# Performance work log

Measured on AMD Instinct MI355X. Metric: run time of the kernel, lower is better.

## Reference

```python
import jax, jax.numpy as jnp
import numpy as np

E, D, H, T = 8, 2048, 5632, 32768  # experts, dim, hidden_dim, total routed tokens


def setup_inputs() -> dict:
    key = jax.random.key(0)
    k_x, k1, k2, k3 = jax.random.split(key, 4)
    x = jax.random.normal(k_x, (T, D), dtype=jnp.float32)
    # trunc_normal init stds per init_weights (approx: plain normal, same scale)
    std = (2.0 / (D * 24)) ** 0.5
    w1 = jax.random.normal(k1, (E, H, D), dtype=jnp.float32) * std
    w2 = jax.random.normal(k2, (E, D, H), dtype=jnp.float32) * std
    w3 = jax.random.normal(k3, (E, H, D), dtype=jnp.float32) * std
    # tokens are pre-sorted by expert; even split 4096 tokens/expert (sums to T)
    num_tokens_per_expert = jnp.full((E,), T // E, dtype=jnp.int32)
    return {"x": x, "w1": w1, "w2": w2, "w3": w3,
            "num_tokens_per_expert": num_tokens_per_expert}


def _grouped_experts(x, w1, w2, w3, counts):
    # Faithful to _run_experts_grouped_mm: grouped GEMMs computed in bf16,
    # SwiGLU activation, cast back to x dtype.
    xb = x.astype(jnp.bfloat16)
    w1b = jnp.transpose(w1.astype(jnp.bfloat16), (0, 2, 1))  # [E, D, H]
    w3b = jnp.transpose(w3.astype(jnp.bfloat16), (0, 2, 1))  # [E, D, H]
    w2b = jnp.transpose(w2.astype(jnp.bfloat16), (0, 2, 1))  # [E, H, D]
    h1 = jax.lax.ragged_dot(xb, w1b, counts)   # [T, H]
    h3 = jax.lax.ragged_dot(xb, w3b, counts)   # [T, H]
    h = jax.nn.silu(h1) * h3                   # fused SwiGLU gate
    out = jax.lax.ragged_dot(h, w2b, counts)   # [T, D]
    return out.astype(x.dtype)


def reference(x, w1, w2, w3, num_tokens_per_expert):
    return _grouped_experts(x, w1, w2, w3, num_tokens_per_expert)
```

## Files before the change

kernel.cpp:

```cpp
#include <hip/hip_runtime.h>
#include <hip/hip_bf16.h>
#include <stdint.h>

#define TT 32768
#define DD 2048
#define HH 5632
#define NE 8

typedef __bf16 bf16;
typedef __bf16 bf16x8 __attribute__((ext_vector_type(8)));
typedef float  f32x4  __attribute__((ext_vector_type(4)));

__device__ __forceinline__ void gl16(const void* g, void* l) {
    __builtin_amdgcn_global_load_lds(
        (const __attribute__((address_space(1))) void*)g,
        (__attribute__((address_space(3))) void*)l, 16, 0, 0);
}
#define VMW(n) asm volatile("s_waitcnt vmcnt(" #n ")" ::: "memory")
#define LGKM0() do { asm volatile("s_waitcnt lgkmcnt(0)" ::: "memory"); \
                     __builtin_amdgcn_sched_barrier(0); } while (0)
#define BARRIER() __builtin_amdgcn_s_barrier()

__device__ __forceinline__ int swz(int off) { return off ^ (((off >> 7) & 3) << 4); }

__device__ __forceinline__ int expert_of(const int* counts, int row0) {
    int base = 0;
    for (int i = 0; i < NE; ++i) { int c = counts[i]; if (row0 < base + c) return i; base += c; }
    return NE - 1;
}

__global__ __launch_bounds__(256)
void k_cvt(const float* __restrict__ in, bf16* __restrict__ out, long n) {
    long i = ((long)blockIdx.x * 256 + threadIdx.x) * 8;
    const long stride = (long)gridDim.x * 256 * 8;
    for (; i < n; i += stride) {
        const float4* p = (const float4*)(in + i);
        float4 a = p[0], b = p[1];
        union { bf16 v[8]; uint4 u; } r;
        r.v[0] = (bf16)a.x; r.v[1] = (bf16)a.y; r.v[2] = (bf16)a.z; r.v[3] = (bf16)a.w;
        r.v[4] = (bf16)b.x; r.v[5] = (bf16)b.y; r.v[6] = (bf16)b.z; r.v[7] = (bf16)b.w;
        *(uint4*)(out + i) = r.u;
    }
}

__global__ __launch_bounds__(512, 2)
void k_moe1(const bf16* __restrict__ xb, const bf16* __restrict__ w1b,
            const bf16* __restrict__ w3b, const int* __restrict__ counts,
            bf16* __restrict__ h) {
    extern __shared__ __align__(16) char sm[];
    const int tid = threadIdx.x;
    const int c = blockIdx.x & 7;
    const int j = blockIdx.x >> 3;
    const int NSEG = 22;

    const int mt = (c << 4) + (j & 15);
    const int row0 = mt * 256;
    const int e = expert_of(counts, row0);

    const int s0 = swz(tid * 16);
    const int s1 = 8192 + s0;
    const int dst0 = tid * 16;

    const char* sa0 = (const char*)xb + (((size_t)(row0 + (s0 >> 6)) * DD) << 1) + (s0 & 63);
    const char* sa1 = (const char*)xb + (((size_t)(row0 + (s1 >> 6)) * DD) << 1) + (s1 & 63);
    const char* w1p = (const char*)(w1b + (size_t)e * HH * DD);
    const char* w3p = (const char*)(w3b + (size_t)e * HH * DD);
    int c0 = (j >> 4) * 128;
    const char* sa2 = w1p + (((size_t)(c0 + (s0 >> 6)) * DD) << 1) + (s0 & 63);
    const char* sa3 = w3p + (((size_t)(c0 + (s0 >> 6)) * DD) << 1) + (s0 & 63);
    const size_t WADV = ((size_t)256 * DD) << 1;

    auto stageA = [&](int ko, int bufb) {
        gl16(sa0 + ko, sm + bufb + dst0);
        gl16(sa1 + ko, sm + bufb + 8192 + dst0);
    };
    auto stageB = [&](int ko, int bufb) {
        gl16(sa2 + ko, sm + bufb + 16384 + dst0);
        gl16(sa3 + ko, sm + bufb + 24576 + dst0);
    };

    const int lane = tid & 63, wv = tid >> 6;
    const int wrow = wv >> 2, wcol = wv & 3;
    const int lrow = lane & 15, kb = (lane >> 4) << 4;
    const int aoff0 = swz((wrow * 128 + lrow) * 64 + kb);
    const int boff0 = swz((wcol * 32 + lrow) * 64 + kb);

    f32x4 acc1[8][2] = {};
    f32x4 acc3[8][2] = {};

    stageA(0, 0);          stageB(0, 0);
    stageA(64, 1 << 15);   stageB(64, 1 << 15);
    stageA(128, 2 << 15);  stageB(128, 2 << 15);
    VMW(8);
    BARRIER();

    int ccol0 = (j >> 4) * 128;
    const int crow = row0 + wrow * 128 + ((lane >> 4) << 2);

    for (int sg = 0; sg < NSEG; ++sg) {
        const bool fin = (sg == NSEG - 1);
        for (int tp = 0; tp < 16; ++tp) {
#pragma unroll
            for (int k = 0; k < 4; ++k) {
                const int t = tp * 4 + k;
                const char* db = sm + (k << 15);
                const int bS = ((k + 3) & 3) << 15;
                const int ko3 = ((t + 3) & 63) << 6;
                bf16x8 af[4], b1[2], b3[2];
#pragma unroll
                for (int mi = 0; mi < 4; ++mi) af[mi] = *(const bf16x8*)(db + aoff0 + mi * 1024);
#pragma unroll
                for (int ni = 0; ni < 2; ++ni) {
                    b1[ni] = *(const bf16x8*)(db + 16384 + boff0 + ni * 1024);
                    b3[ni] = *(const bf16x8*)(db + 24576 + boff0 + ni * 1024);
                }
                if (t == 61 && !fin) { sa2 += WADV; sa3 += WADV; }
                if (!fin || t < 61) stageA(ko3, bS);
                BARRIER();
                LGKM0();
                __builtin_amdgcn_s_setprio(1);
#pragma unroll
                for (int mi = 0; mi < 4; ++mi)
#pragma unroll
                    for (int ni = 0; ni < 2; ++ni) {
                        acc1[mi][ni] = __builtin_amdgcn_mfma_f32_16x16x32_bf16(af[mi], b1[ni], acc1[mi][ni], 0, 0, 0);
                        acc3[mi][ni] = __builtin_amdgcn_mfma_f32_16x16x32_bf16(af[mi], b3[ni], acc3[mi][ni], 0, 0, 0);
                    }
                __builtin_amdgcn_s_setprio(0);
                BARRIER();
                bf16x8 ag[4];
#pragma unroll
                for (int mi = 0; mi < 4; ++mi) ag[mi] = *(const bf16x8*)(db + aoff0 + (mi + 4) * 1024);
                if (!fin || t < 61) { stageB(ko3, bS); VMW(8); }
                else if (t == 61) { VMW(4); }
                else if (t == 62) { VMW(0); }
                BARRIER();
                LGKM0();
                __builtin_amdgcn_s_setprio(1);
#pragma unroll
                for (int mi = 0; mi < 4; ++mi)
#pragma unroll
                    for (int ni = 0; ni < 2; ++ni) {
                        acc1[mi + 4][ni] = __builtin_amdgcn_mfma_f32_16x16x32_bf16(ag[mi], b1[ni], acc1[mi + 4][ni], 0, 0, 0);
                        acc3[mi + 4][ni] = __builtin_amdgcn_mfma_f32_16x16x32_bf16(ag[mi], b3[ni], acc3[mi + 4][ni], 0, 0, 0);
                    }
                __builtin_amdgcn_s_setprio(0);
                BARRIER();
            }
        }
#pragma unroll
        for (int mi = 0; mi < 8; ++mi)
#pragma unroll
            for (int ni = 0; ni < 2; ++ni) {
#pragma unroll
                for (int jj = 0; jj < 4; ++jj) {
                    int row = crow + mi * 16 + jj;
                    int col = ccol0 + wcol * 32 + ni * 16 + lrow;
                    float f1 = (float)(bf16)acc1[mi][ni][jj];
                    float f3 = (float)(bf16)acc3[mi][ni][jj];
                    float s = f1 / (1.0f + __expf(-f1));
                    h[(size_t)row * HH + col] = (bf16)(s * f3);
                }
                acc1[mi][ni] = (f32x4){0.f, 0.f, 0.f, 0.f};
                acc3[mi][ni] = (f32x4){0.f, 0.f, 0.f, 0.f};
            }
        ccol0 += 256;
    }
}

__global__ __launch_bounds__(512, 2)
void k_g2(const bf16* __restrict__ hb, const bf16* __restrict__ w2b,
          const int* __restrict__ counts, float* __restrict__ out) {
    extern __shared__ __align__(16) char sm[];
    const int tid = threadIdx.x;
    const int c = blockIdx.x & 7;
    const int j = blockIdx.x >> 3;
    const int NSEG = 4;
    const int NT = 176;

    const int mt = (c << 4) + (j & 15);
    const int row0 = mt * 256;
    const int e = expert_of(counts, row0);

    const int s0 = swz(tid * 16);
    const int s1 = 8192 + s0;
    const int dst0 = tid * 16;

    const char* sa0 = (const char*)hb + (((size_t)(row0 + (s0 >> 6)) * HH) << 1) + (s0 & 63);
    const char* sa1 = (const char*)hb + (((size_t)(row0 + (s1 >> 6)) * HH) << 1) + (s1 & 63);
    const char* wp = (const char*)(w2b + (size_t)e * DD * HH);
    int c0 = (j >> 4) * 256;
    const char* sa2 = wp + (((size_t)(c0 + (s0 >> 6)) * HH) << 1) + (s0 & 63);
    const char* sa3 = wp + (((size_t)(c0 + (s1 >> 6)) * HH) << 1) + (s1 & 63);
    const size_t WADV = ((size_t)512 * HH) << 1;

    auto stageA = [&](int ko, int bufb) {
        gl16(sa0 + ko, sm + bufb + dst0);
        gl16(sa1 + ko, sm + bufb + 8192 + dst0);
    };
    auto stageB = [&](int ko, int bufb) {
        gl16(sa2 + ko, sm + bufb + 16384 + dst0);
        gl16(sa3 + ko, sm + bufb + 24576 + dst0);
    };

    const int lane = tid & 63, wv = tid >> 6;
    const int wrow = wv >> 2, wcol = wv & 3;
    const int lrow = lane & 15, kb = (lane >> 4) << 4;
    const int aoff0 = swz((wrow * 128 + lrow) * 64 + kb);
    const int boff0 = swz((wcol * 64 + lrow) * 64 + kb);

    f32x4 acc[8][4] = {};

    stageA(0, 0);          stageB(0, 0);
    stageA(64, 1 << 15);   stageB(64, 1 << 15);
    stageA(128, 2 << 15);  stageB(128, 2 << 15);
    VMW(8);
    BARRIER();

    int ccol0 = (j >> 4) * 256;
    const int crow = row0 + wrow * 128 + ((lane >> 4) << 2);

    for (int sg = 0; sg < NSEG; ++sg) {
        const bool fin = (sg == NSEG - 1);
        for (int tp = 0; tp < 44; ++tp) {
#pragma unroll
            for (int k = 0; k < 4; ++k) {
                const int t = tp * 4 + k;
                const char* db = sm + (k << 15);
                const int bS = ((k + 3) & 3) << 15;
                const int t3 = (t + 3 >= NT) ? t + 3 - NT : t + 3;
                const int ko3 = t3 << 6;
                bf16x8 af[4], bf[4];
#pragma unroll
                for (int mi = 0; mi < 4; ++mi) af[mi] = *(const bf16x8*)(db + aoff0 + mi * 1024);
#pragma unroll
                for (int ni = 0; ni < 4; ++ni) bf[ni] = *(const bf16x8*)(db + 16384 + boff0 + ni * 1024);
                if (t == NT - 3 && !fin) { sa2 += WADV; sa3 += WADV; }
                if (!fin || t < NT - 3) stageA(ko3, bS);
                BARRIER();
                LGKM0();
                __builtin_amdgcn_s_setprio(1);
#pragma unroll
                for (int mi = 0; mi < 4; ++mi)
#pragma unroll
                    for (int ni = 0; ni < 4; ++ni)
                        acc[mi][ni] = __builtin_amdgcn_mfma_f32_16x16x32_bf16(af[mi], bf[ni], acc[mi][ni], 0, 0, 0);
                __builtin_amdgcn_s_setprio(0);
                BARRIER();
                bf16x8 ag[4];
#pragma unroll
                for (int mi = 0; mi < 4; ++mi) ag[mi] = *(const bf16x8*)(db + aoff0 + (mi + 4) * 1024);
                if (!fin || t < NT - 3) { stageB(ko3, bS); VMW(8); }
                else if (t == NT - 3) { VMW(4); }
                else if (t == NT - 2) { VMW(0); }
                BARRIER();
                LGKM0();
                __builtin_amdgcn_s_setprio(1);
#pragma unroll
                for (int mi = 0; mi < 4; ++mi)
#pragma unroll
                    for (int ni = 0; ni < 4; ++ni)
                        acc[mi + 4][ni] = __builtin_amdgcn_mfma_f32_16x16x32_bf16(ag[mi], bf[ni], acc[mi + 4][ni], 0, 0, 0);
                __builtin_amdgcn_s_setprio(0);
                BARRIER();
            }
        }
#pragma unroll
        for (int mi = 0; mi < 8; ++mi)
#pragma unroll
            for (int ni = 0; ni < 4; ++ni) {
#pragma unroll
                for (int jj = 0; jj < 4; ++jj) {
                    int row = crow + mi * 16 + jj;
                    int col = ccol0 + wcol * 64 + ni * 16 + lrow;
                    out[(size_t)row * DD + col] = (float)(bf16)acc[mi][ni][jj];
                }
                acc[mi][ni] = (f32x4){0.f, 0.f, 0.f, 0.f};
            }
        ccol0 += 512;
    }
}

extern "C" void kernel_launch(void* const* d_in, const int* in_sizes, int n_in,
                              void* d_out, int out_size, void* d_ws, size_t ws_size,
                              hipStream_t stream) {
    const float* x      = (const float*)d_in[0];
    const float* w1     = (const float*)d_in[1];
    const float* w2     = (const float*)d_in[2];
    const float* w3     = (const float*)d_in[3];
    const int*   counts = (const int*)d_in[4];
    float* out = (float*)d_out;

    const size_t xb_b = (size_t)TT * DD * 2;
    const size_t h_b  = (size_t)TT * HH * 2;
    const size_t w_b  = (size_t)NE * HH * DD * 2;
    const size_t need_full = xb_b + h_b + 2 * w_b;
    if (ws_size < need_full) return;

    bf16* xb  = (bf16*)d_ws;
    bf16* h   = (bf16*)((char*)d_ws + xb_b);
    bf16* wsA = (bf16*)((char*)d_ws + xb_b + h_b);
    bf16* wsB = (bf16*)((char*)d_ws + xb_b + h_b + w_b);

    hipFuncSetAttribute((const void*)k_moe1, hipFuncAttributeMaxDynamicSharedMemorySize, 131072);
    hipFuncSetAttribute((const void*)k_g2,   hipFuncAttributeMaxDynamicSharedMemorySize, 131072);

    k_cvt<<<2048, 256, 0, stream>>>(x,  xb,  (long)TT * DD);
    k_cvt<<<2048, 256, 0, stream>>>(w1, wsA, (long)NE * HH * DD);
    k_cvt<<<2048, 256, 0, stream>>>(w3, wsB, (long)NE * HH * DD);
    k_moe1<<<256, 512, 131072, stream>>>(xb, wsA, wsB, counts, h);
    k_cvt<<<2048, 256, 0, stream>>>(w2, wsA, (long)NE * DD * HH);
    k_g2<<<256, 512, 131072, stream>>>(h, wsA, counts, out);
}
```

Measured before the change: 2.582 ms.

## Fuse w1/w3 fp32-to-bf16 conversion into first GEMM's B-tile staging

Removes the two separate conversion kernels for w1 and w3. The first grouped GEMM now loads fp32 weights into registers two k-steps ahead, converts them to bf16 and writes them into LDS, replacing direct global-to-LDS bf16 loads. This avoids writing and re-reading about 370MB of converted weights. The cost is twice the global bytes per B tile, since each of the 256 blocks rereads fp32 weights, plus extra register pressure and a reworked wait schedule.

```diff
diff --git a/kernel.cpp b/kernel.cpp
--- a/kernel.cpp
+++ b/kernel.cpp
@@ -44,8 +44,8 @@
 }
 
 __global__ __launch_bounds__(512, 2)
-void k_moe1(const bf16* __restrict__ xb, const bf16* __restrict__ w1b,
-            const bf16* __restrict__ w3b, const int* __restrict__ counts,
+void k_moe1(const bf16* __restrict__ xb, const float* __restrict__ w1,
+            const float* __restrict__ w3, const int* __restrict__ counts,
             bf16* __restrict__ h) {
     extern __shared__ __align__(16) char sm[];
     const int tid = threadIdx.x;
@@ -63,20 +63,33 @@
 
     const char* sa0 = (const char*)xb + (((size_t)(row0 + (s0 >> 6)) * DD) << 1) + (s0 & 63);
     const char* sa1 = (const char*)xb + (((size_t)(row0 + (s1 >> 6)) * DD) << 1) + (s1 & 63);
-    const char* w1p = (const char*)(w1b + (size_t)e * HH * DD);
-    const char* w3p = (const char*)(w3b + (size_t)e * HH * DD);
+
     int c0 = (j >> 4) * 128;
-    const char* sa2 = w1p + (((size_t)(c0 + (s0 >> 6)) * DD) << 1) + (s0 & 63);
-    const char* sa3 = w3p + (((size_t)(c0 + (s0 >> 6)) * DD) << 1) + (s0 & 63);
-    const size_t WADV = ((size_t)256 * DD) << 1;
+    const char* w1f = (const char*)w1 + (((size_t)e * HH * DD) << 2)
+                      + (((size_t)(c0 + (s0 >> 6)) * DD) << 2) + ((s0 & 63) << 1);
+    const char* w3f = (const char*)w3 + (((size_t)e * HH * DD) << 2)
+                      + (((size_t)(c0 + (s0 >> 6)) * DD) << 2) + ((s0 & 63) << 1);
+    const size_t WADVf = ((size_t)256 * DD) << 2;
 
     auto stageA = [&](int ko, int bufb) {
         gl16(sa0 + ko, sm + bufb + dst0);
         gl16(sa1 + ko, sm + bufb + 8192 + dst0);
     };
-    auto stageB = [&](int ko, int bufb) {
-        gl16(sa2 + ko, sm + bufb + 16384 + dst0);
-        gl16(sa3 + ko, sm + bufb + 24576 + dst0);
+    auto wfload = [&](int tau, float4& l1a, float4& l1b, float4& l3a, float4& l3b) {
+        const char* p1 = w1f + ((size_t)tau << 7);
+        const char* p3 = w3f + ((size_t)tau << 7);
+        l1a = *(const float4*)(p1);      l1b = *(const float4*)(p1 + 16);
+        l3a = *(const float4*)(p3);      l3b = *(const float4*)(p3 + 16);
+    };
+    auto wfwrite = [&](int bufb, const float4& l1a, const float4& l1b,
+                       const float4& l3a, const float4& l3b) {
+        union { bf16 v[8]; uint4 u; } r1, r3;
+        r1.v[0] = (bf16)l1a.x; r1.v[1] = (bf16)l1a.y; r1.v[2] = (bf16)l1a.z; r1.v[3] = (bf16)l1a.w;
+        r1.v[4] = (bf16)l1b.x; r1.v[5] = (bf16)l1b.y; r1.v[6] = (bf16)l1b.z; r1.v[7] = (bf16)l1b.w;
+        r3.v[0] = (bf16)l3a.x; r3.v[1] = (bf16)l3a.y; r3.v[2] = (bf16)l3a.z; r3.v[3] = (bf16)l3a.w;
+        r3.v[4] = (bf16)l3b.x; r3.v[5] = (bf16)l3b.y; r3.v[6] = (bf16)l3b.z; r3.v[7] = (bf16)l3b.w;
+        *(uint4*)(sm + bufb + 16384 + dst0) = r1.u;
+        *(uint4*)(sm + bufb + 24576 + dst0) = r3.u;
     };
 
     const int lane = tid & 63, wv = tid >> 6;
@@ -87,11 +100,17 @@
 
     f32x4 acc1[8][2] = {};
     f32x4 acc3[8][2] = {};
-
-    stageA(0, 0);          stageB(0, 0);
-    stageA(64, 1 << 15);   stageB(64, 1 << 15);
-    stageA(128, 2 << 15);  stageB(128, 2 << 15);
-    VMW(8);
+    float4 A1a, A1b, A3a, A3b;
+    float4 B1a, B1b, B3a, B3b;
+
+    wfload(0, A1a, A1b, A3a, A3b);
+    wfload(1, B1a, B1b, B3a, B3b);
+    stageA(0, 0); stageA(64, 1 << 15); stageA(128, 2 << 15);
+    VMW(10);
+    __builtin_amdgcn_sched_barrier(0);
+    wfwrite(0, A1a, A1b, A3a, A3b);
+    VMW(4);
+    LGKM0();
     BARRIER();
 
     int ccol0 = (j >> 4) * 128;
@@ -105,7 +124,6 @@
                 const int t = tp * 4 + k;
                 const char* db = sm + (k << 15);
                 const int bS = ((k + 3) & 3) << 15;
-                const int ko3 = ((t + 3) & 63) << 6;
                 bf16x8 af[4], b1[2], b3[2];
 #pragma unroll
                 for (int mi = 0; mi < 4; ++mi) af[mi] = *(const bf16x8*)(db + aoff0 + mi * 1024);
@@ -114,8 +132,12 @@
                     b1[ni] = *(const bf16x8*)(db + 16384 + boff0 + ni * 1024);
                     b3[ni] = *(const bf16x8*)(db + 24576 + boff0 + ni * 1024);
                 }
-                if (t == 61 && !fin) { sa2 += WADV; sa3 += WADV; }
-                if (!fin || t < 61) stageA(ko3, bS);
+                if (t == 62 && !fin) { w1f += WADVf; w3f += WADVf; }
+                if (!fin || t <= 61) {
+                    if ((k & 1) == 0) wfload((t + 2) & 63, A1a, A1b, A3a, A3b);
+                    else              wfload((t + 2) & 63, B1a, B1b, B3a, B3b);
+                }
+                if (!fin || t < 61) stageA(((t + 3) & 63) << 6, bS);
                 BARRIER();
                 LGKM0();
                 __builtin_amdgcn_s_setprio(1);
@@ -131,9 +153,6 @@
                 bf16x8 ag[4];
 #pragma unroll
                 for (int mi = 0; mi < 4; ++mi) ag[mi] = *(const bf16x8*)(db + aoff0 + (mi + 4) * 1024);
-                if (!fin || t < 61) { stageB(ko3, bS); VMW(8); }
-                else if (t == 61) { VMW(4); }
-                else if (t == 62) { VMW(0); }
                 BARRIER();
                 LGKM0();
                 __builtin_amdgcn_s_setprio(1);
@@ -145,6 +164,16 @@
                         acc3[mi + 4][ni] = __builtin_amdgcn_mfma_f32_16x16x32_bf16(ag[mi], b3[ni], acc3[mi + 4][ni], 0, 0, 0);
                     }
                 __builtin_amdgcn_s_setprio(0);
+                if (!fin || t < 61) { VMW(8); }
+                else if (t == 61)   { VMW(6); }
+                else if (t == 62)   { VMW(0); }
+                __builtin_amdgcn_sched_barrier(0);
+                if (!fin || t < 63) {
+                    const int bW = ((k + 1) & 3) << 15;
+                    if (((k + 1) & 1) == 0) wfwrite(bW, A1a, A1b, A3a, A3b);
+                    else                    wfwrite(bW, B1a, B1b, B3a, B3b);
+                    LGKM0();
+                }
                 BARRIER();
             }
         }
@@ -294,21 +323,17 @@
     const size_t xb_b = (size_t)TT * DD * 2;
     const size_t h_b  = (size_t)TT * HH * 2;
     const size_t w_b  = (size_t)NE * HH * DD * 2;
-    const size_t need_full = xb_b + h_b + 2 * w_b;
-    if (ws_size < need_full) return;
+    if (ws_size < xb_b + h_b + w_b) return;
 
     bf16* xb  = (bf16*)d_ws;
     bf16* h   = (bf16*)((char*)d_ws + xb_b);
     bf16* wsA = (bf16*)((char*)d_ws + xb_b + h_b);
-    bf16* wsB = (bf16*)((char*)d_ws + xb_b + h_b + w_b);
 
     hipFuncSetAttribute((const void*)k_moe1, hipFuncAttributeMaxDynamicSharedMemorySize, 131072);
     hipFuncSetAttribute((const void*)k_g2,   hipFuncAttributeMaxDynamicSharedMemorySize, 131072);
 
     k_cvt<<<2048, 256, 0, stream>>>(x,  xb,  (long)TT * DD);
-    k_cvt<<<2048, 256, 0, stream>>>(w1, wsA, (long)NE * HH * DD);
-    k_cvt<<<2048, 256, 0, stream>>>(w3, wsB, (long)NE * HH * DD);
-    k_moe1<<<256, 512, 131072, stream>>>(xb, wsA, wsB, counts, h);
+    k_moe1<<<256, 512, 131072, stream>>>(xb, w1, w3, counts, h);
     k_cvt<<<2048, 256, 0, stream>>>(w2, wsA, (long)NE * DD * HH);
     k_g2<<<256, 512, 131072, stream>>>(h, wsA, counts, out);
 }
```

Measured after the change: 3.279 ms. +27.0%, slower.

## Fuse input conversions into one kernel and overlap w2 conversion with GEMM1

Applied to the files above, without the earlier changes.

Merges the three fp32-to-bf16 conversions for x, w1 and w3 into a single launch. When the workspace has room for a third weight buffer, the w2 conversion moves inside the first grouped GEMM kernel: each block converts a slice of w2 between MFMA phases. This hides the memory-bound w2 conversion behind compute and removes a separate launch. The cost is extra global traffic and instructions inside the GEMM main loop, plus a larger workspace requirement. If the workspace is too small it falls back to the old path.

```diff
diff --git a/kernel.cpp b/kernel.cpp
--- a/kernel.cpp
+++ b/kernel.cpp
@@ -29,8 +29,8 @@
     return NE - 1;
 }
 
-__global__ __launch_bounds__(256)
-void k_cvt(const float* __restrict__ in, bf16* __restrict__ out, long n) {
+__device__ __forceinline__ void cvt_range(const float* __restrict__ in,
+                                          bf16* __restrict__ out, long n) {
     long i = ((long)blockIdx.x * 256 + threadIdx.x) * 8;
     const long stride = (long)gridDim.x * 256 * 8;
     for (; i < n; i += stride) {
@@ -43,10 +43,25 @@
     }
 }
 
+__global__ __launch_bounds__(256)
+void k_cvt(const float* __restrict__ in, bf16* __restrict__ out, long n) {
+    cvt_range(in, out, n);
+}
+
+__global__ __launch_bounds__(256)
+void k_cvt3(const float* __restrict__ x,  bf16* __restrict__ xb,
+            const float* __restrict__ w1, bf16* __restrict__ w1b,
+            const float* __restrict__ w3, bf16* __restrict__ w3b) {
+    cvt_range(x,  xb,  (long)TT * DD);
+    cvt_range(w1, w1b, (long)NE * HH * DD);
+    cvt_range(w3, w3b, (long)NE * HH * DD);
+}
+
 __global__ __launch_bounds__(512, 2)
 void k_moe1(const bf16* __restrict__ xb, const bf16* __restrict__ w1b,
             const bf16* __restrict__ w3b, const int* __restrict__ counts,
-            bf16* __restrict__ h) {
+            bf16* __restrict__ h,
+            const float* __restrict__ w2f, bf16* __restrict__ w2o) {
     extern __shared__ __align__(16) char sm[];
     const int tid = threadIdx.x;
     const int c = blockIdx.x & 7;
@@ -70,6 +85,9 @@
     const char* sa3 = w3p + (((size_t)(c0 + (s0 >> 6)) * DD) << 1) + (s0 & 63);
     const size_t WADV = ((size_t)256 * DD) << 1;
 
+    const size_t gbase = (size_t)blockIdx.x * 352;
+    const bool docvt = (w2f != nullptr);
+
     auto stageA = [&](int ko, int bufb) {
         gl16(sa0 + ko, sm + bufb + dst0);
         gl16(sa1 + ko, sm + bufb + 8192 + dst0);
@@ -145,6 +163,13 @@
                         acc3[mi + 4][ni] = __builtin_amdgcn_mfma_f32_16x16x32_bf16(ag[mi], b3[ni], acc3[mi + 4][ni], 0, 0, 0);
                     }
                 __builtin_amdgcn_s_setprio(0);
+                if (k == 0 && docvt) {
+                    const size_t g = gbase + (size_t)sg * 16 + tp;
+                    const float2 v = *(const float2*)((const char*)w2f + (g << 12) + ((size_t)tid << 3));
+                    union { bf16 hv[2]; uint32_t u; } r;
+                    r.hv[0] = (bf16)v.x; r.hv[1] = (bf16)v.y;
+                    *(uint32_t*)((char*)w2o + (g << 11) + ((size_t)tid << 2)) = r.u;
+                }
                 BARRIER();
             }
         }
@@ -294,8 +319,9 @@
     const size_t xb_b = (size_t)TT * DD * 2;
     const size_t h_b  = (size_t)TT * HH * 2;
     const size_t w_b  = (size_t)NE * HH * DD * 2;
-    const size_t need_full = xb_b + h_b + 2 * w_b;
-    if (ws_size < need_full) return;
+    const size_t need_base  = xb_b + h_b + 2 * w_b;
+    const size_t need_fused = xb_b + h_b + 3 * w_b;
+    if (ws_size < need_base) return;
 
     bf16* xb  = (bf16*)d_ws;
     bf16* h   = (bf16*)((char*)d_ws + xb_b);
@@ -305,10 +331,15 @@
     hipFuncSetAttribute((const void*)k_moe1, hipFuncAttributeMaxDynamicSharedMemorySize, 131072);
     hipFuncSetAttribute((const void*)k_g2,   hipFuncAttributeMaxDynamicSharedMemorySize, 131072);
 
-    k_cvt<<<2048, 256, 0, stream>>>(x,  xb,  (long)TT * DD);
-    k_cvt<<<2048, 256, 0, stream>>>(w1, wsA, (long)NE * HH * DD);
-    k_cvt<<<2048, 256, 0, stream>>>(w3, wsB, (long)NE * HH * DD);
-    k_moe1<<<256, 512, 131072, stream>>>(xb, wsA, wsB, counts, h);
-    k_cvt<<<2048, 256, 0, stream>>>(w2, wsA, (long)NE * DD * HH);
-    k_g2<<<256, 512, 131072, stream>>>(h, wsA, counts, out);
-}
+    if (ws_size >= need_fused) {
+        bf16* w2b = (bf16*)((char*)d_ws + xb_b + h_b + 2 * w_b);
+        k_cvt3<<<2048, 256, 0, stream>>>(x, xb, w1, wsA, w3, wsB);
+        k_moe1<<<256, 512, 131072, stream>>>(xb, wsA, wsB, counts, h, w2, w2b);
+        k_g2<<<256, 512, 131072, stream>>>(h, w2b, counts, out);
+    } else {
+        k_cvt3<<<2048, 256, 0, stream>>>(x, xb, w1, wsA, w3, wsB);
+        k_moe1<<<256, 512, 131072, stream>>>(xb, wsA, wsB, counts, h, nullptr, nullptr);
+        k_cvt<<<2048, 256, 0, stream>>>(w2, wsA, (long)NE * DD * HH);
+        k_g2<<<256, 512, 131072, stream>>>(h, wsA, counts, out);
+    }
+}
```

After: 2.649 ms. 1.03x slower.
